# Kernel tuning notes

Hardware: AMD Instinct MI355X
Metric: run time of the kernel (lower is better)

Reference implementation:

```python
import jax, jax.numpy as jnp
import numpy as np

TEMPERATURE = 0.5


def setup_inputs() -> dict:
    key = jax.random.key(0)
    k1, k2, k3, k4 = jax.random.split(key, 4)
    B, D = 4096, 256
    return {
        "emb_i": jax.random.normal(k1, (B, D), dtype=jnp.float32),
        "emb_j": jax.random.normal(k2, (B, D), dtype=jnp.float32),
        "tags": jax.random.randint(k3, (B,), 0, 100, dtype=jnp.int32),
        "num_classes": 100,
        "document_ids": jax.random.randint(k4, (B,), 0, 512, dtype=jnp.int32),
    }


def reference(emb_i, emb_j, tags, num_classes, document_ids):
    # L2-normalize rows (cosine similarity of normalized vectors == dot product)
    z_i = emb_i / jnp.linalg.norm(emb_i, axis=1, keepdims=True)
    z_j = emb_j / jnp.linalg.norm(emb_j, axis=1, keepdims=True)
    reps = jnp.concatenate([z_i, z_j], axis=0)          # [2B, D]
    sim = reps @ reps.T                                  # [2B, 2B]
    exp_sim = jnp.exp(sim / TEMPERATURE)                 # [2B, 2B]

    # sum(square(onehot_j - onehot_i))/2 == 1.0 iff labels differ, else 0.0
    tags2 = jnp.concatenate([tags, tags], axis=0)        # [2B]
    docs2 = jnp.concatenate([document_ids, document_ids], axis=0)
    mask = ((tags2[:, None] != tags2[None, :]) & (docs2[:, None] != docs2[None, :])).astype(exp_sim.dtype)

    denom = jnp.sum(mask * exp_sim, axis=1) + 0.1        # [2B]

    B = tags.shape[0]
    idx = jnp.arange(2 * B)
    pair = jnp.concatenate([jnp.arange(B) + B, jnp.arange(B)])  # partner index of each row
    numerator = exp_sim[idx, pair]                       # [2B]

    loss = jnp.sum(-jnp.log(numerator / denom)) / (2 * B)
    return loss
```

## Files before the change

kernel.cpp:

```cpp
#include <hip/hip_runtime.h>
#include <hip/hip_bf16.h>
#include <cstdint>
#include <cstddef>

#define B_ROWS 4096
#define D_DIM  256
#define TWOB   8192
static constexpr float kScale = 2.8853900817779268f;

typedef __bf16 bf16_t;
typedef __bf16 bf16x4 __attribute__((ext_vector_type(4)));
typedef __bf16 bf16x8 __attribute__((ext_vector_type(8)));
typedef float  f32x4  __attribute__((ext_vector_type(4)));

#define WS_Z    0ull
#define WS_KEYS ((size_t)TWOB * D_DIM * 2)
#define WS_DEN  (WS_KEYS + (size_t)TWOB * 4)
#define WS_PAIR (WS_DEN + (size_t)TWOB * 4)


__global__ __launch_bounds__(256) void prep_kernel(
    const float* __restrict__ emb_i, const float* __restrict__ emb_j,
    const int* __restrict__ tags, const int* __restrict__ docs,
    bf16_t* __restrict__ Z, int* __restrict__ keys,
    float* __restrict__ denom, float* __restrict__ pair)
{
  __shared__ float4 zbuf[4][64];
  const int t = threadIdx.x;
  const int lane = t & 63, w = t >> 6;
  const int b = blockIdx.x;
  const int rlocal = 2 * b + (w & 1);
  const int row = rlocal + (w >> 1) * B_ROWS;
  const float* src = (w >> 1) ? (emb_j + (size_t)rlocal * D_DIM)
                              : (emb_i + (size_t)rlocal * D_DIM);
  float4 v = *(const float4*)(src + lane * 4);
  float ss = v.x * v.x + v.y * v.y + v.z * v.z + v.w * v.w;
  #pragma unroll
  for (int m = 32; m; m >>= 1) ss += __shfl_xor(ss, m, 64);
  float inv = 1.0f / sqrtf(ss);
  float4 z = {v.x * inv, v.y * inv, v.z * inv, v.w * inv};
  zbuf[w][lane] = z;

  bf16x4 q;
  q[0] = (bf16_t)z.x; q[1] = (bf16_t)z.y; q[2] = (bf16_t)z.z; q[3] = (bf16_t)z.w;
  int chunk = lane >> 4;
  int g     = (lane >> 1) & 7;
  int gs    = g ^ (row & 7);
  int half  = lane & 1;
  *(bf16x4*)(Z + (size_t)row * D_DIM + chunk * 64 + gs * 8 + half * 4) = q;

  if (lane == 0) {
    keys[row] = (tags[rlocal] << 16) | docs[rlocal];
    denom[row] = 0.f;
  }
  __syncthreads();
  if (w < 2) {
    float4 a = zbuf[w][lane], c = zbuf[w + 2][lane];
    float d = a.x * c.x + a.y * c.y + a.z * c.z + a.w * c.w;
    #pragma unroll
    for (int m = 32; m; m >>= 1) d += __shfl_xor(d, m, 64);
    if (lane == 0) pair[2 * b + w] = d;
  }
}

#define BM 128
#define BK 64
#define NKT (D_DIM / BK)
#define STRIP 2

__global__ __launch_bounds__(256, 2) void fused_kernel(
    const bf16_t* __restrict__ Z, const int* __restrict__ keys,
    float* __restrict__ denom)
{
  __shared__ bf16_t sA[2][BM * BK];
  __shared__ bf16_t sB[2][BM * BK];
  const int tid  = threadIdx.x;
  const int lane = tid & 63;
  const int w    = tid >> 6;
  const int wr = w >> 1, wc = w & 1;
  const int l15 = lane & 15, l4 = lane >> 4;

  int t0 = 2 * blockIdx.x;
  int rt0 = (int)((sqrtf(8.0f * (float)t0 + 1.0f) - 1.0f) * 0.5f);
  while ((rt0 + 1) * (rt0 + 2) / 2 <= t0) ++rt0;
  while (rt0 * (rt0 + 1) / 2 > t0) --rt0;
  int ct0 = t0 - rt0 * (rt0 + 1) / 2;
  int rt1 = (ct0 < rt0) ? rt0 : rt0 + 1;
  int ct1 = (ct0 < rt0) ? ct0 + 1 : 0;

  const int  r0s[2] = {rt0 * BM, rt1 * BM};
  const int  c0s[2] = {ct0 * BM, ct1 * BM};
  const bool od[2]  = {rt0 != ct0, rt1 != ct1};

  f32x4 acc[4][4];
  const f32x4 vzero = {0.f, 0.f, 0.f, 0.f};
  #pragma unroll
  for (int mi = 0; mi < 4; ++mi)
    #pragma unroll
    for (int ni = 0; ni < 4; ++ni) acc[mi][ni] = vzero;

  auto STAGE = [&](int buf, int ti, int kt) {
    #pragma unroll
    for (int i = 0; i < 4; ++i) {
      int o  = i * 4096 + tid * 16;
      int rl = o >> 7, ob = o & 127;
      const bf16_t* ga = Z + (size_t)(r0s[ti] + rl) * D_DIM + kt * 64 + (ob >> 1);
      __builtin_amdgcn_global_load_lds(
          (const __attribute__((address_space(1))) void*)ga,
          (__attribute__((address_space(3))) void*)((char*)&sA[buf][0] + o), 16, 0, 0);
      const bf16_t* gb = Z + (size_t)(c0s[ti] + rl) * D_DIM + kt * 64 + (ob >> 1);
      __builtin_amdgcn_global_load_lds(
          (const __attribute__((address_space(1))) void*)gb,
          (__attribute__((address_space(3))) void*)((char*)&sB[buf][0] + o), 16, 0, 0);
    }
  };

  auto EPI = [&](int ti) {
    const int row0 = r0s[ti], col0 = c0s[ti];
    int keyr[4][4];
    #pragma unroll
    for (int mi = 0; mi < 4; ++mi)
      #pragma unroll
      for (int j = 0; j < 4; ++j)
        keyr[mi][j] = keys[row0 + wr * 64 + mi * 16 + l4 * 4 + j];
    int keyc[4];
    #pragma unroll
    for (int ni = 0; ni < 4; ++ni)
      keyc[ni] = keys[col0 + wc * 64 + ni * 16 + l15];

    float rowsum[4][4];
    #pragma unroll
    for (int mi = 0; mi < 4; ++mi)
      #pragma unroll
      for (int j = 0; j < 4; ++j) rowsum[mi][j] = 0.f;
    float colsum[4] = {0.f, 0.f, 0.f, 0.f};

    #pragma unroll
    for (int ni = 0; ni < 4; ++ni) {
      #pragma unroll
      for (int mi = 0; mi < 4; ++mi) {
        #pragma unroll
        for (int j = 0; j < 4; ++j) {
          int x = keyr[mi][j] ^ keyc[ni];
          bool m = ((x >> 16) != 0) & ((x & 0xFFFF) != 0);
          float e = m ? __builtin_amdgcn_exp2f(acc[mi][ni][j] * kScale) : 0.f;
          rowsum[mi][j] += e;
          colsum[ni] += e;
        }
      }
    }
    #pragma unroll
    for (int mi = 0; mi < 4; ++mi)
      #pragma unroll
      for (int j = 0; j < 4; ++j) {
        float v = rowsum[mi][j];
        v += __shfl_xor(v, 1, 64);
        v += __shfl_xor(v, 2, 64);
        v += __shfl_xor(v, 4, 64);
        v += __shfl_xor(v, 8, 64);
        if (l15 == 0)
          atomicAdd(&denom[row0 + wr * 64 + mi * 16 + l4 * 4 + j], v);
      }
    if (od[ti]) {
      #pragma unroll
      for (int ni = 0; ni < 4; ++ni) {
        float v = colsum[ni];
        v += __shfl_xor(v, 16, 64);
        v += __shfl_xor(v, 32, 64);
        if (l4 == 0)
          atomicAdd(&denom[col0 + wc * 64 + ni * 16 + l15], v);
      }
    }
    #pragma unroll
    for (int mi = 0; mi < 4; ++mi)
      #pragma unroll
      for (int ni = 0; ni < 4; ++ni) acc[mi][ni] = vzero;
  };

  STAGE(0, 0, 0);
  #pragma unroll
  for (int s = 0; s < STRIP * NKT; ++s) {
    const int buf = s & 1;
    __syncthreads();
    if (s < STRIP * NKT - 1) STAGE(buf ^ 1, (s + 1) >> 2, (s + 1) & 3);

    bf16x8 af[2][4], bfr[2][4];
    #pragma unroll
    for (int h = 0; h < 2; ++h) {
      #pragma unroll
      for (int mi = 0; mi < 4; ++mi) {
        int rl  = wr * 64 + mi * 16 + l15;
        int gsa = (h * 4 + l4) ^ (rl & 7);
        af[h][mi] = *(const bf16x8*)(&sA[buf][rl * 64 + gsa * 8]);
        int cl  = wc * 64 + mi * 16 + l15;
        int gsb = (h * 4 + l4) ^ (cl & 7);
        bfr[h][mi] = *(const bf16x8*)(&sB[buf][cl * 64 + gsb * 8]);
      }
    }
    #pragma unroll
    for (int h = 0; h < 2; ++h)
      #pragma unroll
      for (int mi = 0; mi < 4; ++mi)
        #pragma unroll
        for (int ni = 0; ni < 4; ++ni)
          acc[mi][ni] = __builtin_amdgcn_mfma_f32_16x16x32_bf16(
              af[h][mi], bfr[h][ni], acc[mi][ni], 0, 0, 0);
    __syncthreads();
    if ((s & 3) == 3) EPI(s >> 2);
  }
}

__global__ __launch_bounds__(1024) void tail_kernel(
    const float* __restrict__ denom, const float* __restrict__ pair,
    float* __restrict__ out)
{
  const int t = threadIdx.x;
  const int lane = t & 63, w = t >> 6;
  float c = 0.f;
  #pragma unroll
  for (int i = 0; i < 8; ++i) c += __logf(denom[t + 1024 * i] + 0.1f);
  #pragma unroll
  for (int i = 0; i < 4; ++i) c -= 4.0f * pair[t + 1024 * i];
  #pragma unroll
  for (int m = 32; m; m >>= 1) c += __shfl_xor(c, m, 64);
  __shared__ float red[16];
  if (lane == 0) red[w] = c;
  __syncthreads();
  if (t == 0) {
    float s = 0.f;
    #pragma unroll
    for (int i = 0; i < 16; ++i) s += red[i];
    out[0] = s * (1.0f / (float)TWOB);
  }
}

extern "C" void kernel_launch(void* const* d_in, const int* in_sizes, int n_in,
                              void* d_out, int out_size, void* d_ws, size_t ws_size,
                              hipStream_t stream) {
  const float* emb_i = (const float*)d_in[0];
  const float* emb_j = (const float*)d_in[1];
  const int*   tags  = (const int*)d_in[2];
  const int*   docs  = (const int*)d_in[4];

  char* ws = (char*)d_ws;
  bf16_t* Z     = (bf16_t*)(ws + WS_Z);
  int*    keys  = (int*)(ws + WS_KEYS);
  float*  denom = (float*)(ws + WS_DEN);
  float*  pair  = (float*)(ws + WS_PAIR);
  float*  out   = (float*)d_out;

  prep_kernel<<<B_ROWS / 2, 256, 0, stream>>>(emb_i, emb_j, tags, docs, Z, keys, denom, pair);
  const int ntiles = (TWOB / BM) * (TWOB / BM + 1) / 2;
  fused_kernel<<<ntiles / STRIP, 256, 0, stream>>>(Z, keys, denom);
  tail_kernel<<<1, 1024, 0, stream>>>(denom, pair, out);
}
```

Measured before the change: 122.7 us.

## Fuse tail reduction into GEMM kernel, enlarge strips, use finer-grained barriers

Each block of the fused kernel now covers four triangle tiles instead of two, which halves the block count to 520, and blocks are remapped across XCDs with a modulo-8 swizzle. The per-step __syncthreads pair becomes raw s_barrier with explicit vmcnt waits, so the next stage's global-to-LDS loads can stay in flight. The separate tail kernel is removed: a global atomic counter lets the last-finishing block compute the log-sum loss, saving one launch. The risks are lower parallelism with fewer blocks, and correctness that depends on the hand-written waitcnt and on atomic visibility of denom.

```diff
diff --git a/kernel.cpp b/kernel.cpp
--- a/kernel.cpp
+++ b/kernel.cpp
@@ -17,13 +17,14 @@
 #define WS_KEYS ((size_t)TWOB * D_DIM * 2)
 #define WS_DEN  (WS_KEYS + (size_t)TWOB * 4)
 #define WS_PAIR (WS_DEN + (size_t)TWOB * 4)
+#define WS_CNT  (WS_PAIR + (size_t)B_ROWS * 4)
 
 
 __global__ __launch_bounds__(256) void prep_kernel(
     const float* __restrict__ emb_i, const float* __restrict__ emb_j,
     const int* __restrict__ tags, const int* __restrict__ docs,
     bf16_t* __restrict__ Z, int* __restrict__ keys,
-    float* __restrict__ denom, float* __restrict__ pair)
+    float* __restrict__ denom, float* __restrict__ pair, int* __restrict__ cnt)
 {
   __shared__ float4 zbuf[4][64];
   const int t = threadIdx.x;
@@ -53,6 +54,7 @@
     keys[row] = (tags[rlocal] << 16) | docs[rlocal];
     denom[row] = 0.f;
   }
+  if (b == 0 && t == 0) cnt[0] = 0;
   __syncthreads();
   if (w < 2) {
     float4 a = zbuf[w][lane], c = zbuf[w + 2][lane];
@@ -66,31 +68,39 @@
 #define BM 128
 #define BK 64
 #define NKT (D_DIM / BK)
-#define STRIP 2
+#define STRIP 4
+#define TOT (STRIP * NKT)
+#define NBLK 520
 
 __global__ __launch_bounds__(256, 2) void fused_kernel(
     const bf16_t* __restrict__ Z, const int* __restrict__ keys,
-    float* __restrict__ denom)
+    float* __restrict__ denom, const float* __restrict__ pair,
+    int* __restrict__ cnt, float* __restrict__ out)
 {
   __shared__ bf16_t sA[2][BM * BK];
   __shared__ bf16_t sB[2][BM * BK];
+  __shared__ int s_last;
+  __shared__ float s_red[4];
   const int tid  = threadIdx.x;
   const int lane = tid & 63;
   const int w    = tid >> 6;
   const int wr = w >> 1, wc = w & 1;
   const int l15 = lane & 15, l4 = lane >> 4;
 
-  int t0 = 2 * blockIdx.x;
-  int rt0 = (int)((sqrtf(8.0f * (float)t0 + 1.0f) - 1.0f) * 0.5f);
-  while ((rt0 + 1) * (rt0 + 2) / 2 <= t0) ++rt0;
-  while (rt0 * (rt0 + 1) / 2 > t0) --rt0;
-  int ct0 = t0 - rt0 * (rt0 + 1) / 2;
-  int rt1 = (ct0 < rt0) ? rt0 : rt0 + 1;
-  int ct1 = (ct0 < rt0) ? ct0 + 1 : 0;
-
-  const int  r0s[2] = {rt0 * BM, rt1 * BM};
-  const int  c0s[2] = {ct0 * BM, ct1 * BM};
-  const bool od[2]  = {rt0 != ct0, rt1 != ct1};
+  const int bid = (blockIdx.x % 8) * (NBLK / 8) + blockIdx.x / 8;
+
+  int t0 = 4 * bid;
+  int rt = (int)((sqrtf(8.0f * (float)t0 + 1.0f) - 1.0f) * 0.5f);
+  while ((rt + 1) * (rt + 2) / 2 <= t0) ++rt;
+  while (rt * (rt + 1) / 2 > t0) --rt;
+  int ct = t0 - rt * (rt + 1) / 2;
+  int r0s[STRIP], c0s[STRIP];
+  bool od[STRIP];
+  #pragma unroll
+  for (int i = 0; i < STRIP; ++i) {
+    r0s[i] = rt * BM; c0s[i] = ct * BM; od[i] = (rt != ct);
+    if (++ct > rt) { ++rt; ct = 0; }
+  }
 
   f32x4 acc[4][4];
   const f32x4 vzero = {0.f, 0.f, 0.f, 0.f};
@@ -179,10 +189,17 @@
 
   STAGE(0, 0, 0);
   #pragma unroll
-  for (int s = 0; s < STRIP * NKT; ++s) {
+  for (int s = 0; s < TOT; ++s) {
     const int buf = s & 1;
-    __syncthreads();
-    if (s < STRIP * NKT - 1) STAGE(buf ^ 1, (s + 1) >> 2, (s + 1) & 3);
+    __builtin_amdgcn_s_barrier();
+    if (s + 1 < TOT) {
+      STAGE(buf ^ 1, (s + 1) >> 2, (s + 1) & 3);
+      asm volatile("s_waitcnt vmcnt(8)" ::: "memory");
+    } else {
+      asm volatile("s_waitcnt vmcnt(0)" ::: "memory");
+    }
+    __builtin_amdgcn_s_barrier();
+    __builtin_amdgcn_sched_barrier(0);
 
     bf16x8 af[2][4], bfr[2][4];
     #pragma unroll
@@ -205,32 +222,32 @@
         for (int ni = 0; ni < 4; ++ni)
           acc[mi][ni] = __builtin_amdgcn_mfma_f32_16x16x32_bf16(
               af[h][mi], bfr[h][ni], acc[mi][ni], 0, 0, 0);
+
+    if ((s & 3) == 3) EPI(s >> 2);
+  }
+
+  __syncthreads();
+  if (tid == 0) {
+    int done = __hip_atomic_fetch_add(cnt, 1, __ATOMIC_ACQ_REL, __HIP_MEMORY_SCOPE_AGENT);
+    s_last = (done == NBLK - 1) ? 1 : 0;
+  }
+  __syncthreads();
+  if (s_last) {
+    float c = 0.f;
+    #pragma unroll
+    for (int i = 0; i < 32; ++i) {
+      float d = __hip_atomic_load(&denom[i * 256 + tid], __ATOMIC_RELAXED,
+                                  __HIP_MEMORY_SCOPE_AGENT);
+      c += __logf(d + 0.1f);
+    }
+    #pragma unroll
+    for (int i = 0; i < 16; ++i) c -= 4.0f * pair[i * 256 + tid];
+    #pragma unroll
+    for (int m = 32; m; m >>= 1) c += __shfl_xor(c, m, 64);
+    if (lane == 0) s_red[w] = c;
     __syncthreads();
-    if ((s & 3) == 3) EPI(s >> 2);
-  }
-}
-
-__global__ __launch_bounds__(1024) void tail_kernel(
-    const float* __restrict__ denom, const float* __restrict__ pair,
-    float* __restrict__ out)
-{
-  const int t = threadIdx.x;
-  const int lane = t & 63, w = t >> 6;
-  float c = 0.f;
-  #pragma unroll
-  for (int i = 0; i < 8; ++i) c += __logf(denom[t + 1024 * i] + 0.1f);
-  #pragma unroll
-  for (int i = 0; i < 4; ++i) c -= 4.0f * pair[t + 1024 * i];
-  #pragma unroll
-  for (int m = 32; m; m >>= 1) c += __shfl_xor(c, m, 64);
-  __shared__ float red[16];
-  if (lane == 0) red[w] = c;
-  __syncthreads();
-  if (t == 0) {
-    float s = 0.f;
-    #pragma unroll
-    for (int i = 0; i < 16; ++i) s += red[i];
-    out[0] = s * (1.0f / (float)TWOB);
+    if (tid == 0)
+      out[0] = (s_red[0] + s_red[1] + s_red[2] + s_red[3]) * (1.0f / (float)TWOB);
   }
 }
 
@@ -247,10 +264,9 @@
   int*    keys  = (int*)(ws + WS_KEYS);
   float*  denom = (float*)(ws + WS_DEN);
   float*  pair  = (float*)(ws + WS_PAIR);
+  int*    cnt   = (int*)(ws + WS_CNT);
   float*  out   = (float*)d_out;
 
-  prep_kernel<<<B_ROWS / 2, 256, 0, stream>>>(emb_i, emb_j, tags, docs, Z, keys, denom, pair);
-  const int ntiles = (TWOB / BM) * (TWOB / BM + 1) / 2;
-  fused_kernel<<<ntiles / STRIP, 256, 0, stream>>>(Z, keys, denom);
-  tail_kernel<<<1, 1024, 0, stream>>>(denom, pair, out);
+  prep_kernel<<<B_ROWS / 2, 256, 0, stream>>>(emb_i, emb_j, tags, docs, Z, keys, denom, pair, cnt);
+  fused_kernel<<<NBLK, 256, 0, stream>>>(Z, keys, denom, pair, cnt, out);
 }
```

Result: slower. 144.0 us (+17.4%).
